# Kernel tuning notes

Hardware: AMD Instinct MI355X
Metric: run time of the kernel (lower is better)

Reference implementation:

```python
import jax, jax.numpy as jnp
import numpy as np

MOMENTUM = 0.99
EPS = 1e-08


def setup_inputs() -> dict:
    key = jax.random.key(0)
    k1, = jax.random.split(key, 1)
    B, F, T = 32, 257, 3000
    mag = jax.random.uniform(k1, (B, F, T), dtype=jnp.float32)  # magnitudes >= 0
    bias = jnp.zeros((1,), dtype=jnp.float32)
    running_mean = jnp.ones((1,), dtype=jnp.float32)
    return {"mag": mag, "bias": bias, "running_mean": running_mean}


def reference(mag, bias, running_mean):
    """Causal per-frame EMA energy normalization (eval-mode sequence path).

    mag: [B, F, T] -> (mag_norm [B, F, T], mag_mean [B, 1, T])
    """
    B, F, T = mag.shape
    frame_means = mag.mean(axis=1)          # [B, T]
    init = jnp.broadcast_to(running_mean, (B,))  # m_0 = running_mean per batch

    def step(carry, fm_t):
        m = MOMENTUM * carry + (1.0 - MOMENTUM) * fm_t  # [B]
        return m, m

    _, means = jax.lax.scan(step, init, frame_means.T)  # means: [T, B]
    mean_with_bias = means.T + bias[0]                  # [B, T]
    mag_norm = mag / (mean_with_bias[:, None, :] + EPS)  # [B, F, T]
    mag_mean = mean_with_bias[:, None, :]               # [B, 1, T]
    return mag_norm, mag_mean
```

## Files before the change

### kernel.cpp

```cpp
#include <hip/hip_runtime.h>


#define B_  32
#define F_  257
#define T_  3000
#define T4  750
#define NCH 32
#define MOM 0.99f
#define OMM 0.01f
#define EPS_ 1e-8f

__global__ __launch_bounds__(256) void k0_zero(float4* __restrict__ fs4) {
    int i = blockIdx.x * 256 + threadIdx.x;
    if (i < B_ * T4) fs4[i] = make_float4(0.f, 0.f, 0.f, 0.f);
}

__global__ __launch_bounds__(256) void k1_rowsum(const float* __restrict__ mag,
                                                 float* __restrict__ framesum) {
    const int blk = blockIdx.x;
    const int b   = blk >> 5;
    const int c   = blk & (NCH - 1);
    const int f0  = (c * F_) >> 5;
    const int f1  = ((c + 1) * F_) >> 5;
    const int tid = threadIdx.x;
    const float4* magv = reinterpret_cast<const float4*>(mag);

    float4 a0 = make_float4(0.f, 0.f, 0.f, 0.f);
    float4 a1 = a0, a2 = a0;
    const bool has2 = tid < (T4 - 512);

    int base = (b * F_ + f0) * T4;
    for (int f = f0; f < f1; ++f, base += T4) {
        float4 v0 = magv[base + tid];
        float4 v1 = magv[base + tid + 256];
        a0.x += v0.x; a0.y += v0.y; a0.z += v0.z; a0.w += v0.w;
        a1.x += v1.x; a1.y += v1.y; a1.z += v1.z; a1.w += v1.w;
        if (has2) {
            float4 v2 = magv[base + tid + 512];
            a2.x += v2.x; a2.y += v2.y; a2.z += v2.z; a2.w += v2.w;
        }
    }
    float* fs = framesum + b * T_;
    int t = tid * 4;
    __hip_atomic_fetch_add(fs + t,     a0.x, __ATOMIC_RELAXED, __HIP_MEMORY_SCOPE_AGENT);
    __hip_atomic_fetch_add(fs + t + 1, a0.y, __ATOMIC_RELAXED, __HIP_MEMORY_SCOPE_AGENT);
    __hip_atomic_fetch_add(fs + t + 2, a0.z, __ATOMIC_RELAXED, __HIP_MEMORY_SCOPE_AGENT);
    __hip_atomic_fetch_add(fs + t + 3, a0.w, __ATOMIC_RELAXED, __HIP_MEMORY_SCOPE_AGENT);
    t += 1024;
    __hip_atomic_fetch_add(fs + t,     a1.x, __ATOMIC_RELAXED, __HIP_MEMORY_SCOPE_AGENT);
    __hip_atomic_fetch_add(fs + t + 1, a1.y, __ATOMIC_RELAXED, __HIP_MEMORY_SCOPE_AGENT);
    __hip_atomic_fetch_add(fs + t + 2, a1.z, __ATOMIC_RELAXED, __HIP_MEMORY_SCOPE_AGENT);
    __hip_atomic_fetch_add(fs + t + 3, a1.w, __ATOMIC_RELAXED, __HIP_MEMORY_SCOPE_AGENT);
    if (has2) {
        t += 1024;
        __hip_atomic_fetch_add(fs + t,     a2.x, __ATOMIC_RELAXED, __HIP_MEMORY_SCOPE_AGENT);
        __hip_atomic_fetch_add(fs + t + 1, a2.y, __ATOMIC_RELAXED, __HIP_MEMORY_SCOPE_AGENT);
        __hip_atomic_fetch_add(fs + t + 2, a2.z, __ATOMIC_RELAXED, __HIP_MEMORY_SCOPE_AGENT);
        __hip_atomic_fetch_add(fs + t + 3, a2.w, __ATOMIC_RELAXED, __HIP_MEMORY_SCOPE_AGENT);
    }
}

__global__ __launch_bounds__(256) void k2_scan_norm(const float* __restrict__ framesum,
                                                    const float* __restrict__ bias,
                                                    const float* __restrict__ rmean,
                                                    const float* __restrict__ mag,
                                                    float* __restrict__ out,
                                                    float* __restrict__ mag_mean) {
    __shared__ float4 xs4[T4];
    float* xs = reinterpret_cast<float*>(xs4);
    __shared__ float sA[256];
    __shared__ float sB[256];

    const int blk = blockIdx.x;
    const int b   = blk >> 5;
    const int c   = blk & (NCH - 1);
    const int f0  = (c * F_) >> 5;
    const int f1  = ((c + 1) * F_) >> 5;
    const int tid = threadIdx.x;

    {
        const float4* fsv = reinterpret_cast<const float4*>(framesum) + b * T4;
        const float inv_f = 1.0f / F_;
        for (int i = tid; i < T4; i += 256) {
            float4 v = fsv[i];
            v.x *= inv_f; v.y *= inv_f; v.z *= inv_f; v.w *= inv_f;
            xs4[i] = v;
        }
    }
    __syncthreads();

    const int CH = 12;
    const int t0 = tid * CH;
    float A = 1.f, Bv = 0.f;
    if (t0 < T_) {
        #pragma unroll
        for (int j = 0; j < CH; ++j) {
            Bv = MOM * Bv + OMM * xs[t0 + j];
            A *= MOM;
        }
    }
    sA[tid] = A; sB[tid] = Bv;
    __syncthreads();

    for (int off = 1; off < 256; off <<= 1) {
        float cA = sA[tid], cB = sB[tid];
        float pA = 1.f, pB = 0.f;
        if (tid >= off) { pA = sA[tid - off]; pB = sB[tid - off]; }
        __syncthreads();
        if (tid >= off) { sA[tid] = pA * cA; sB[tid] = pB * cA + cB; }
        __syncthreads();
    }

    float pA = 1.f, pB = 0.f;
    if (tid > 0) { pA = sA[tid - 1]; pB = sB[tid - 1]; }
    __syncthreads();

    const float bias0 = bias[0];
    if (t0 < T_) {
        float m = pA * rmean[0] + pB;
        #pragma unroll
        for (int j = 0; j < CH; ++j) {
            m = MOM * m + OMM * xs[t0 + j];
            xs[t0 + j] = m + bias0;
        }
    }
    __syncthreads();

    if (c == 0) {
        for (int i = tid; i < T4; i += 256)
            reinterpret_cast<float4*>(mag_mean + b * T_)[i] = xs4[i];
    }
    for (int i = tid; i < T4; i += 256) {
        float4 v = xs4[i];
        v.x = 1.0f / (v.x + EPS_); v.y = 1.0f / (v.y + EPS_);
        v.z = 1.0f / (v.z + EPS_); v.w = 1.0f / (v.w + EPS_);
        xs4[i] = v;
    }
    __syncthreads();

    const float4* magv = reinterpret_cast<const float4*>(mag);
    float4* ov = reinterpret_cast<float4*>(out);
    const bool has2 = tid < (T4 - 512);
    const float4 r0 = xs4[tid];
    const float4 r1 = xs4[tid + 256];
    const float4 r2 = has2 ? xs4[tid + 512] : r0;
    int base = (b * F_ + f0) * T4;
    for (int f = f0; f < f1; ++f, base += T4) {
        float4 v0 = magv[base + tid];
        float4 v1 = magv[base + tid + 256];
        float4 o;
        o.x = v0.x * r0.x; o.y = v0.y * r0.y; o.z = v0.z * r0.z; o.w = v0.w * r0.w;
        ov[base + tid] = o;
        o.x = v1.x * r1.x; o.y = v1.y * r1.y; o.z = v1.z * r1.z; o.w = v1.w * r1.w;
        ov[base + tid + 256] = o;
        if (has2) {
            float4 v2 = magv[base + tid + 512];
            o.x = v2.x * r2.x; o.y = v2.y * r2.y; o.z = v2.z * r2.z; o.w = v2.w * r2.w;
            ov[base + tid + 512] = o;
        }
    }
}

extern "C" void kernel_launch(void* const* d_in, const int* in_sizes, int n_in,
                              void* d_out, int out_size, void* d_ws, size_t ws_size,
                              hipStream_t stream) {
    const float* mag   = (const float*)d_in[0];
    const float* bias  = (const float*)d_in[1];
    const float* rmean = (const float*)d_in[2];
    float* out      = (float*)d_out;
    float* mag_mean = out + (size_t)B_ * F_ * T_;
    float* framesum = (float*)d_ws;

    k0_zero<<<(B_ * T4 + 255) / 256, 256, 0, stream>>>((float4*)framesum);
    k1_rowsum<<<B_ * NCH, 256, 0, stream>>>(mag, framesum);
    k2_scan_norm<<<B_ * NCH, 256, 0, stream>>>(framesum, bias, rmean, mag, out, mag_mean);
}
```

Measured before the change: 234.6 us.

## Replace atomic frame-sum reduction with per-segment block reduction over time

The zero-fill kernel and the atomic-add row-sum kernel are replaced by one kernel that splits each batch's time axis into 25 segments of 30 float4 columns. Each block sums all 257 frequency rows for its segment using 8 row groups, then combines the groups in shared memory and writes the frame sums directly. This removes one launch and the global atomics. In exchange only 240 of 256 threads do work, and reads are narrower (30 float4 per row stride), which may hurt coalescing and memory-level parallelism.

```diff
diff --git a/kernel.cpp b/kernel.cpp
--- a/kernel.cpp
+++ b/kernel.cpp
@@ -1,62 +1,50 @@
 #include <hip/hip_runtime.h>
 
 
-#define B_  32
-#define F_  257
-#define T_  3000
-#define T4  750
-#define NCH 32
+#define B_   32
+#define F_   257
+#define T_   3000
+#define T4   750
+#define NSEG 25
+#define SEG4 30
+#define NCH  32
 #define MOM 0.99f
 #define OMM 0.01f
 #define EPS_ 1e-8f
 
-__global__ __launch_bounds__(256) void k0_zero(float4* __restrict__ fs4) {
-    int i = blockIdx.x * 256 + threadIdx.x;
-    if (i < B_ * T4) fs4[i] = make_float4(0.f, 0.f, 0.f, 0.f);
-}
+__global__ __launch_bounds__(256) void k1_seg(const float* __restrict__ mag,
+                                              float* __restrict__ framesum) {
+    __shared__ float4 red[8][SEG4];
+    const int blk = blockIdx.x;
+    const int b   = blk / NSEG;
+    const int s   = blk % NSEG;
+    const int tid = threadIdx.x;
+    const int g    = tid / SEG4;
+    const int slot = tid % SEG4;
 
-__global__ __launch_bounds__(256) void k1_rowsum(const float* __restrict__ mag,
-                                                 float* __restrict__ framesum) {
-    const int blk = blockIdx.x;
-    const int b   = blk >> 5;
-    const int c   = blk & (NCH - 1);
-    const int f0  = (c * F_) >> 5;
-    const int f1  = ((c + 1) * F_) >> 5;
-    const int tid = threadIdx.x;
-    const float4* magv = reinterpret_cast<const float4*>(mag);
+    if (g < 8) {
+        const float4* magv = reinterpret_cast<const float4*>(mag);
+        const int col = s * SEG4 + slot;
+        float4 a = make_float4(0.f, 0.f, 0.f, 0.f);
+        int idx = (b * F_ + g) * T4 + col;
+        const int step = 8 * T4;
+        #pragma unroll 4
+        for (int f = g; f < F_; f += 8, idx += step) {
+            float4 v = magv[idx];
+            a.x += v.x; a.y += v.y; a.z += v.z; a.w += v.w;
+        }
+        red[g][slot] = a;
+    }
+    __syncthreads();
 
-    float4 a0 = make_float4(0.f, 0.f, 0.f, 0.f);
-    float4 a1 = a0, a2 = a0;
-    const bool has2 = tid < (T4 - 512);
-
-    int base = (b * F_ + f0) * T4;
-    for (int f = f0; f < f1; ++f, base += T4) {
-        float4 v0 = magv[base + tid];
-        float4 v1 = magv[base + tid + 256];
-        a0.x += v0.x; a0.y += v0.y; a0.z += v0.z; a0.w += v0.w;
-        a1.x += v1.x; a1.y += v1.y; a1.z += v1.z; a1.w += v1.w;
-        if (has2) {
-            float4 v2 = magv[base + tid + 512];
-            a2.x += v2.x; a2.y += v2.y; a2.z += v2.z; a2.w += v2.w;
+    if (tid < SEG4) {
+        float4 a = red[0][tid];
+        #pragma unroll
+        for (int gg = 1; gg < 8; ++gg) {
+            float4 v = red[gg][tid];
+            a.x += v.x; a.y += v.y; a.z += v.z; a.w += v.w;
         }
-    }
-    float* fs = framesum + b * T_;
-    int t = tid * 4;
-    __hip_atomic_fetch_add(fs + t,     a0.x, __ATOMIC_RELAXED, __HIP_MEMORY_SCOPE_AGENT);
-    __hip_atomic_fetch_add(fs + t + 1, a0.y, __ATOMIC_RELAXED, __HIP_MEMORY_SCOPE_AGENT);
-    __hip_atomic_fetch_add(fs + t + 2, a0.z, __ATOMIC_RELAXED, __HIP_MEMORY_SCOPE_AGENT);
-    __hip_atomic_fetch_add(fs + t + 3, a0.w, __ATOMIC_RELAXED, __HIP_MEMORY_SCOPE_AGENT);
-    t += 1024;
-    __hip_atomic_fetch_add(fs + t,     a1.x, __ATOMIC_RELAXED, __HIP_MEMORY_SCOPE_AGENT);
-    __hip_atomic_fetch_add(fs + t + 1, a1.y, __ATOMIC_RELAXED, __HIP_MEMORY_SCOPE_AGENT);
-    __hip_atomic_fetch_add(fs + t + 2, a1.z, __ATOMIC_RELAXED, __HIP_MEMORY_SCOPE_AGENT);
-    __hip_atomic_fetch_add(fs + t + 3, a1.w, __ATOMIC_RELAXED, __HIP_MEMORY_SCOPE_AGENT);
-    if (has2) {
-        t += 1024;
-        __hip_atomic_fetch_add(fs + t,     a2.x, __ATOMIC_RELAXED, __HIP_MEMORY_SCOPE_AGENT);
-        __hip_atomic_fetch_add(fs + t + 1, a2.y, __ATOMIC_RELAXED, __HIP_MEMORY_SCOPE_AGENT);
-        __hip_atomic_fetch_add(fs + t + 2, a2.z, __ATOMIC_RELAXED, __HIP_MEMORY_SCOPE_AGENT);
-        __hip_atomic_fetch_add(fs + t + 3, a2.w, __ATOMIC_RELAXED, __HIP_MEMORY_SCOPE_AGENT);
+        reinterpret_cast<float4*>(framesum)[b * T4 + s * SEG4 + tid] = a;
     }
 }
 
@@ -171,7 +159,6 @@
     float* mag_mean = out + (size_t)B_ * F_ * T_;
     float* framesum = (float*)d_ws;
 
-    k0_zero<<<(B_ * T4 + 255) / 256, 256, 0, stream>>>((float4*)framesum);
-    k1_rowsum<<<B_ * NCH, 256, 0, stream>>>(mag, framesum);
+    k1_seg<<<B_ * NSEG, 256, 0, stream>>>(mag, framesum);
     k2_scan_norm<<<B_ * NCH, 256, 0, stream>>>(framesum, bias, rmean, mag, out, mag_mean);
 }
```

Result: faster. 196.1 us (-16.4%).
